# Kernel tuning notes

Hardware: AMD Instinct MI355X
Metric: run time of the kernel (lower is better)

Reference implementation:

```python
import jax, jax.numpy as jnp
import numpy as np

D_MODEL = 1024
NUM_HEADS = 16
HEAD_DIM = D_MODEL // NUM_HEADS
ALPHA = 1.0


def setup_inputs() -> dict:
    key = jax.random.key(0)
    ks = jax.random.split(key, 9)
    B, T, D = 2, 2048, D_MODEL
    s = 1.0 / np.sqrt(D)
    inp = {
        "x": jax.random.normal(ks[0], (B, T, D), dtype=jnp.float32),
        "Wq": jax.random.uniform(ks[1], (D, D), jnp.float32, -s, s),
        "bq": jax.random.uniform(ks[2], (D,), jnp.float32, -s, s),
        "Wk": jax.random.uniform(ks[3], (D, D), jnp.float32, -s, s),
        "bk": jax.random.uniform(ks[4], (D,), jnp.float32, -s, s),
        "Wv": jax.random.uniform(ks[5], (D, D), jnp.float32, -s, s),
        "bv": jax.random.uniform(ks[6], (D,), jnp.float32, -s, s),
        "Wo": jax.random.uniform(ks[7], (D, D), jnp.float32, -s, s),
        "bo": jax.random.uniform(ks[8], (D,), jnp.float32, -s, s),
    }
    return inp


def reference(x, Wq, bq, Wk, bk, Wv, bv, Wo, bo):
    B, T, D = x.shape
    H, hd = NUM_HEADS, HEAD_DIM

    def split_heads(y):  # [B,T,D] -> [B,H,T,hd]
        return y.reshape(B, T, H, hd).transpose(0, 2, 1, 3)

    Q = split_heads(x @ Wq.T + bq)
    K = split_heads(x @ Wk.T + bk)
    V = split_heads(x @ Wv.T + bv)

    scores = jnp.einsum('bhid,bhjd->bhij', Q, K) / jnp.sqrt(jnp.float32(hd))

    t = jnp.arange(T)
    delta = t[:, None] - t[None, :]  # [T,T], i - j
    causal_mask = delta < 0          # j > i (strict upper triangle)
    # similarity_power_law decay bias: -(delta)^alpha for delta >= 0, else 0
    decay = jnp.where(causal_mask, 0.0, -(delta.astype(jnp.float32) ** ALPHA))

    scores = jnp.where(causal_mask, -jnp.inf, scores) + decay
    attn = jax.nn.softmax(scores, axis=-1)

    out = jnp.einsum('bhij,bhjd->bhid', attn, V)
    out = out.transpose(0, 2, 1, 3).reshape(B, T, D)
    return out @ Wo.T + bo
```

## Files before the change

### kernel.cpp

```cpp
#include <hip/hip_runtime.h>

#define TT 2048
#define DD 1024
#define HH 16
#define HD 64

typedef __bf16 bf16x8 __attribute__((ext_vector_type(8)));
typedef short short4v __attribute__((ext_vector_type(4)));
typedef float f32x4 __attribute__((ext_vector_type(4)));
typedef unsigned short ushort8v __attribute__((ext_vector_type(8)));

__device__ __forceinline__ unsigned short f2bf(float f) {
  unsigned u = __float_as_uint(f);
  u += 0x7fffu + ((u >> 16) & 1u);
  return (unsigned short)(u >> 16);
}

#if __has_builtin(__builtin_amdgcn_mfma_f32_16x16x16bf16_1k)
__device__ __forceinline__ f32x4 mfma16(short4v a, short4v b, f32x4 c) {
  return __builtin_amdgcn_mfma_f32_16x16x16bf16_1k(a, b, c, 0, 0, 0);
}
#else
__device__ __forceinline__ f32x4 mfma16(short4v a, short4v b, f32x4 c) {
  asm("v_mfma_f32_16x16x16_bf16 %0, %1, %2, %0\n\ts_nop 7\n\ts_nop 7"
      : "+v"(c) : "v"(a), "v"(b));
  return c;
}
#endif

typedef void __attribute__((address_space(1))) as1_void;
typedef void __attribute__((address_space(3))) as3_void;
__device__ __forceinline__ void gl_lds16(const void* g, void* l) {
  __builtin_amdgcn_global_load_lds((as1_void*)g, (as3_void*)l, 16, 0, 0);
}

__global__ __launch_bounds__(256)
void wcmha_cast_all(const float4* __restrict__ x,  const float4* __restrict__ wq,
                    const float4* __restrict__ wk, const float4* __restrict__ wv,
                    const float4* __restrict__ wo,
                    ushort8v* __restrict__ xb,  ushort8v* __restrict__ wqb,
                    ushort8v* __restrict__ wkb, ushort8v* __restrict__ wvb,
                    ushort8v* __restrict__ wob) {
  const int i = blockIdx.x * 256 + threadIdx.x;
  const float4* src;
  ushort8v* dst;
  int off;
  if (i < 524288) {
    src = x; dst = xb; off = i;
  } else {
    int j = i - 524288;
    int sel = j >> 17;
    off = j & 131071;
    const float4* ws_[4] = {wq, wk, wv, wo};
    ushort8v* wd_[4] = {wqb, wkb, wvb, wob};
    src = ws_[sel]; dst = wd_[sel];
  }
  float4 a = src[off * 2];
  float4 b = src[off * 2 + 1];
  ushort8v o;
  o[0] = f2bf(a.x); o[1] = f2bf(a.y); o[2] = f2bf(a.z); o[3] = f2bf(a.w);
  o[4] = f2bf(b.x); o[5] = f2bf(b.y); o[6] = f2bf(b.z); o[7] = f2bf(b.w);
  dst[off] = o;
}

template <int BN_, bool SWAP>
__device__ __forceinline__ void gemm_db(const unsigned short* __restrict__ X,
                                        const unsigned short* __restrict__ W,
                                        int m0, int n0,
                                        unsigned short* As, unsigned short* Bs,
                                        f32x4 acc[4][BN_ / 32]) {
  constexpr int NI = BN_ / 32;
  constexpr int JB = (BN_ * 4) / 256;
  const int tid = threadIdx.x, wid = tid >> 6, lane = tid & 63;
  const int m = lane & 15, quad = lane >> 4;
  const int wm = (wid >> 1) * 64, wn = (wid & 1) * (BN_ / 2);
  const int xq = (quad ^ ((m >> 1) & 3)) * 8;

  const unsigned short* gA[2];
  const unsigned short* gB[JB];
#pragma unroll
  for (int j = 0; j < 2; ++j) {
    int c = wid * 64 + lane + j * 256;
    gA[j] = X + (size_t)(m0 + (c >> 2)) * DD + ((c & 3) ^ ((c >> 3) & 3)) * 8;
  }
#pragma unroll
  for (int j = 0; j < JB; ++j) {
    int c = wid * 64 + lane + j * 256;
    gB[j] = W + (size_t)(n0 + (c >> 2)) * DD + ((c & 3) ^ ((c >> 3) & 3)) * 8;
  }
  unsigned short* lA[2][2];
  unsigned short* lB[2][JB];
#pragma unroll
  for (int p = 0; p < 2; ++p) {
#pragma unroll
    for (int j = 0; j < 2; ++j)
      lA[p][j] = As + p * (128 * 32) + (wid * 64 + j * 256) * 8;
#pragma unroll
    for (int j = 0; j < JB; ++j)
      lB[p][j] = Bs + p * (BN_ * 32) + (wid * 64 + j * 256) * 8;
  }

#pragma unroll
  for (int i = 0; i < 4; ++i)
#pragma unroll
    for (int j = 0; j < NI; ++j) acc[i][j] = (f32x4){0.f, 0.f, 0.f, 0.f};

#pragma unroll
  for (int j = 0; j < 2; ++j) gl_lds16(gA[j], lA[0][j]);
#pragma unroll
  for (int j = 0; j < JB; ++j) gl_lds16(gB[j], lB[0][j]);

  for (int k = 0; k < 32; ++k) {
    const int p = k & 1;
    __syncthreads();
    if (k < 31) {
      const int k1 = (k + 1) * 32;
#pragma unroll
      for (int j = 0; j < 2; ++j) gl_lds16(gA[j] + k1, lA[p ^ 1][j]);
#pragma unroll
      for (int j = 0; j < JB; ++j) gl_lds16(gB[j] + k1, lB[p ^ 1][j]);
    }
    const unsigned short* ap = As + p * (128 * 32);
    const unsigned short* bp = Bs + p * (BN_ * 32);
    bf16x8 af[4], bf[NI];
#pragma unroll
    for (int mi = 0; mi < 4; ++mi)
      af[mi] = *(const bf16x8*)&ap[(wm + mi * 16 + m) * 32 + xq];
#pragma unroll
    for (int ni = 0; ni < NI; ++ni)
      bf[ni] = *(const bf16x8*)&bp[(wn + ni * 16 + m) * 32 + xq];
#pragma unroll
    for (int mi = 0; mi < 4; ++mi)
#pragma unroll
      for (int ni = 0; ni < NI; ++ni)
        acc[mi][ni] = SWAP
            ? __builtin_amdgcn_mfma_f32_16x16x32_bf16(bf[ni], af[mi], acc[mi][ni], 0, 0, 0)
            : __builtin_amdgcn_mfma_f32_16x16x32_bf16(af[mi], bf[ni], acc[mi][ni], 0, 0, 0);
  }
}

__global__ __launch_bounds__(512, 2)
void wcmha_qkv8(const unsigned short* __restrict__ X,
                const unsigned short* __restrict__ WQKV,
                const float* __restrict__ bq, const float* __restrict__ bk,
                const float* __restrict__ bv,
                unsigned short* __restrict__ Qb,
                unsigned short* __restrict__ Kb,
                unsigned short* __restrict__ Vt) {
  __shared__ unsigned short As[2 * 2 * 256 * 32];
  __shared__ unsigned short Bs[2 * 2 * 256 * 32];
  const int tid = threadIdx.x;
  const int lane = tid & 63, wid = tid >> 6;
  const int m = lane & 15, quad = lane >> 4;
  const int wr = wid >> 2, wc = wid & 3;

  const int mt = blockIdx.x & 15, nt = blockIdx.x >> 4;
  const int m0 = mt * 256;
  const int mat = nt >> 2;
  const int n0w = nt * 256;
  const int n0l = (nt & 3) * 256;

  const int srow = tid >> 2;
  const int schunk = ((tid & 3) ^ ((tid >> 3) & 3)) * 8;
  const unsigned short* gA0 = X + (size_t)(m0 + srow) * DD + schunk;
  const unsigned short* gA1 = gA0 + (size_t)128 * DD;
  const unsigned short* gB0 = WQKV + (size_t)(n0w + srow) * DD + schunk;
  const unsigned short* gB1 = gB0 + (size_t)128 * DD;
  const int ldst = tid * 8;

#define SA(buf, ks, koff)                                                     \
  {                                                                           \
    gl_lds16(gA0 + (koff), &As[((buf) * 2 + (ks)) * 8192 + ldst]);            \
    gl_lds16(gA1 + (koff), &As[((buf) * 2 + (ks)) * 8192 + 4096 + ldst]);     \
  }
#define SB(buf, ks, koff)                                                     \
  {                                                                           \
    gl_lds16(gB0 + (koff), &Bs[((buf) * 2 + (ks)) * 8192 + ldst]);            \
    gl_lds16(gB1 + (koff), &Bs[((buf) * 2 + (ks)) * 8192 + 4096 + ldst]);     \
  }

  f32x4 acc[8][4];
#pragma unroll
  for (int i = 0; i < 8; ++i)
#pragma unroll
    for (int j = 0; j < 4; ++j) acc[i][j] = (f32x4){0.f, 0.f, 0.f, 0.f};

  SA(0, 0, 0) SB(0, 0, 0)
  SA(0, 1, 32) SB(0, 1, 32)
  SA(1, 0, 64) SB(1, 0, 64)

  const int xq = (quad ^ ((m >> 1) & 3)) * 8;
  const int arow = wr * 128 + m;
  const int brow = wc * 64 + m;

#pragma unroll 1
  for (int kt = 0; kt < 16; ++kt) {
    const int cur = kt & 1, nxt = cur ^ 1;
    const unsigned short* a0 = &As[(cur * 2 + 0) * 8192];
    const unsigned short* b0 = &Bs[(cur * 2 + 0) * 8192];
    const unsigned short* a1 = &As[(cur * 2 + 1) * 8192];
    const unsigned short* b1 = &Bs[(cur * 2 + 1) * 8192];
    bf16x8 af[8], bf[4];

    if (kt < 15) { asm volatile("s_waitcnt vmcnt(8)" ::: "memory"); }
    else         { asm volatile("s_waitcnt vmcnt(4)" ::: "memory"); }
    __builtin_amdgcn_s_barrier();
    __builtin_amdgcn_sched_barrier(0);
#pragma unroll
    for (int mi = 0; mi < 8; ++mi)
      af[mi] = *(const bf16x8*)&a0[(arow + mi * 16) * 32 + xq];
#pragma unroll
    for (int ni = 0; ni < 4; ++ni)
      bf[ni] = *(const bf16x8*)&b0[(brow + ni * 16) * 32 + xq];
    if (kt < 15) { const int kA = (kt + 1) * 64 + 32; SA(nxt, 1, kA) SB(nxt, 1, kA) }
    __builtin_amdgcn_s_setprio(1);
#pragma unroll
    for (int mi = 0; mi < 8; ++mi)
#pragma unroll
      for (int ni = 0; ni < 4; ++ni)
        acc[mi][ni] = __builtin_amdgcn_mfma_f32_16x16x32_bf16(bf[ni], af[mi], acc[mi][ni], 0, 0, 0);
    __builtin_amdgcn_s_setprio(0);

    if (kt < 15) { asm volatile("s_waitcnt vmcnt(8)" ::: "memory"); }
    else         { asm volatile("s_waitcnt vmcnt(0)" ::: "memory"); }
    __builtin_amdgcn_s_barrier();
    __builtin_amdgcn_sched_barrier(0);
#pragma unroll
    for (int mi = 0; mi < 8; ++mi)
      af[mi] = *(const bf16x8*)&a1[(arow + mi * 16) * 32 + xq];
#pragma unroll
    for (int ni = 0; ni < 4; ++ni)
      bf[ni] = *(const bf16x8*)&b1[(brow + ni * 16) * 32 + xq];
    if (kt < 14) { const int kB = (kt + 2) * 64; SA(cur, 0, kB) SB(cur, 0, kB) }
    __builtin_amdgcn_s_setprio(1);
#pragma unroll
    for (int mi = 0; mi < 8; ++mi)
#pragma unroll
      for (int ni = 0; ni < 4; ++ni)
        acc[mi][ni] = __builtin_amdgcn_mfma_f32_16x16x32_bf16(bf[ni], af[mi], acc[mi][ni], 0, 0, 0);
    __builtin_amdgcn_s_setprio(0);
  }
#undef SA
#undef SB

  if (mat < 2) {
    const float* bias = mat ? bk : bq;
    unsigned short* dst = mat ? Kb : Qb;
#pragma unroll
    for (int mi = 0; mi < 8; ++mi) {
      int row = m0 + wr * 128 + mi * 16 + m;
      int b = row >> 11, t = row & (TT - 1);
#pragma unroll
      for (int ni = 0; ni < 4; ++ni) {
        int col0 = n0l + wc * 64 + ni * 16 + quad * 4;
        int h = col0 >> 6, d0 = col0 & 63;
        float4 bb = *(const float4*)&bias[col0];
        short4v v;
        v[0] = (short)f2bf(acc[mi][ni][0] + bb.x);
        v[1] = (short)f2bf(acc[mi][ni][1] + bb.y);
        v[2] = (short)f2bf(acc[mi][ni][2] + bb.z);
        v[3] = (short)f2bf(acc[mi][ni][3] + bb.w);
        *(short4v*)&dst[((size_t)(b * HH + h) * TT + t) * HD + d0] = v;
      }
    }
  } else {
#pragma unroll
    for (int mi = 0; mi < 8; ++mi) {
      int row = m0 + wr * 128 + mi * 16 + m;
      int b = row >> 11, t = row & (TT - 1);
#pragma unroll
      for (int ni = 0; ni < 4; ++ni) {
        int col0 = n0l + wc * 64 + ni * 16 + quad * 4;
        int h = col0 >> 6, d0 = col0 & 63;
#pragma unroll
        for (int r = 0; r < 4; ++r) {
          float bb = bv[col0 + r];
          Vt[((size_t)(b * HH + h) * HD + d0 + r) * TT + t] =
              f2bf(acc[mi][ni][r] + bb);
        }
      }
    }
  }
}

__global__ __launch_bounds__(256)
void wcmha_gemm_out(const unsigned short* __restrict__ X,
                    const unsigned short* __restrict__ W,
                    const float* __restrict__ bias,
                    float* __restrict__ Y) {
  __shared__ unsigned short As[2 * 128 * 32];
  __shared__ unsigned short Bs[2 * 64 * 32];
  const int m0 = blockIdx.x * 128;
  const int n0 = blockIdx.y * 64;
  const int lane = threadIdx.x & 63, wid = threadIdx.x >> 6;
  const int m = lane & 15, quad = lane >> 4;
  const int wm = (wid >> 1) * 64, wn = (wid & 1) * 32;

  f32x4 acc[4][2];
  gemm_db<64, true>(X, W, m0, n0, As, Bs, acc);

#pragma unroll
  for (int mi = 0; mi < 4; ++mi) {
    int row = m0 + wm + mi * 16 + m;
#pragma unroll
    for (int ni = 0; ni < 2; ++ni) {
      int col0 = n0 + wn + ni * 16 + quad * 4;
      float4 bb = *(const float4*)&bias[col0];
      float4 o;
      o.x = acc[mi][ni][0] + bb.x;
      o.y = acc[mi][ni][1] + bb.y;
      o.z = acc[mi][ni][2] + bb.z;
      o.w = acc[mi][ni][3] + bb.w;
      *(float4*)&Y[(size_t)row * DD + col0] = o;
    }
  }
}

__global__ __launch_bounds__(256)
void wcmha_attn(const unsigned short* __restrict__ Qb,
                const unsigned short* __restrict__ Kb,
                const unsigned short* __restrict__ Vt,
                unsigned short* __restrict__ O) {
  const int wid = threadIdx.x >> 6, lane = threadIdx.x & 63;
  const int gw = (blockIdx.x << 2) + wid;
  const int qt = gw & 127, bh = gw >> 7;
  const int qbase = qt << 4;
  const int il = lane & 15, quad = lane >> 4;
  const int ig = qbase + il;

  const unsigned short* q_ptr = Qb + (size_t)bh * TT * HD;
  const unsigned short* k_ptr = Kb + (size_t)bh * TT * HD;
  const unsigned short* v_ptr = Vt + (size_t)bh * HD * TT;

  const bf16x8 qf0 = *(const bf16x8*)(q_ptr + (size_t)ig * HD + quad * 8);
  const bf16x8 qf1 = *(const bf16x8*)(q_ptr + (size_t)ig * HD + 32 + quad * 8);

  const int j0 = (qbase >= 32) ? qbase - 32 : 0;

  f32x4 st[3];
#pragma unroll
  for (int jt = 0; jt < 3; ++jt) {
    const unsigned short* kp = k_ptr + (size_t)(j0 + jt * 16 + il) * HD;
    bf16x8 k0 = *(const bf16x8*)(kp + quad * 8);
    bf16x8 k1 = *(const bf16x8*)(kp + 32 + quad * 8);
    f32x4 a = {0.f, 0.f, 0.f, 0.f};
    a = __builtin_amdgcn_mfma_f32_16x16x32_bf16(k0, qf0, a, 0, 0, 0);
    a = __builtin_amdgcn_mfma_f32_16x16x32_bf16(k1, qf1, a, 0, 0, 0);
    st[jt] = a;
  }

  float mloc = -3.0e38f;
#pragma unroll
  for (int jt = 0; jt < 3; ++jt)
#pragma unroll
    for (int r = 0; r < 4; ++r) {
      int jg = j0 + jt * 16 + quad * 4 + r;
      float v = (jg > ig) ? -3.0e38f : st[jt][r] * 0.125f - (float)(ig - jg);
      st[jt][r] = v;
      mloc = fmaxf(mloc, v);
    }
  mloc = fmaxf(mloc, __shfl_xor(mloc, 16));
  mloc = fmaxf(mloc, __shfl_xor(mloc, 32));

  float rs = 0.f;
  short4v pf[3];
#pragma unroll
  for (int jt = 0; jt < 3; ++jt)
#pragma unroll
    for (int r = 0; r < 4; ++r) {
      float p = __expf(st[jt][r] - mloc);
      rs += p;
      pf[jt][r] = (short)f2bf(p);
    }
  rs += __shfl_xor(rs, 16);
  rs += __shfl_xor(rs, 32);

  f32x4 o_acc[4];
#pragma unroll
  for (int nt = 0; nt < 4; ++nt) o_acc[nt] = (f32x4){0.f, 0.f, 0.f, 0.f};
#pragma unroll
  for (int jt = 0; jt < 3; ++jt)
#pragma unroll
    for (int nt = 0; nt < 4; ++nt) {
      short4v vf = *(const short4v*)(v_ptr + (size_t)(nt * 16 + il) * TT +
                                     j0 + jt * 16 + quad * 4);
      o_acc[nt] = mfma16(vf, pf[jt], o_acc[nt]);
    }

  const float inv_l = 1.f / rs;
  const int b = bh >> 4, hh = bh & 15;
  unsigned short* ob = O + ((size_t)(b * TT + ig)) * DD + hh * HD;
#pragma unroll
  for (int nt = 0; nt < 4; ++nt) {
    short4v v;
#pragma unroll
    for (int r = 0; r < 4; ++r) v[r] = (short)f2bf(o_acc[nt][r] * inv_l);
    *(short4v*)&ob[nt * 16 + quad * 4] = v;
  }
}

extern "C" void kernel_launch(void* const* d_in, const int* in_sizes, int n_in,
                              void* d_out, int out_size, void* d_ws, size_t ws_size,
                              hipStream_t stream) {
  const float* x  = (const float*)d_in[0];
  const float* Wq = (const float*)d_in[1];
  const float* bq = (const float*)d_in[2];
  const float* Wk = (const float*)d_in[3];
  const float* bk = (const float*)d_in[4];
  const float* Wv = (const float*)d_in[5];
  const float* bv = (const float*)d_in[6];
  const float* Wo = (const float*)d_in[7];
  const float* bo = (const float*)d_in[8];

  char* ws = (char*)d_ws;
  unsigned short* xb  = (unsigned short*)(ws);
  unsigned short* wqb = (unsigned short*)(ws + (8u << 20));
  unsigned short* wkb = wqb + (1u << 20);
  unsigned short* wvb = wkb + (1u << 20);
  unsigned short* wob = wvb + (1u << 20);
  unsigned short* Qb  = (unsigned short*)(ws + (16u << 20));
  unsigned short* Kb  = (unsigned short*)(ws + (24u << 20));
  unsigned short* Vt  = (unsigned short*)(ws + (32u << 20));
  unsigned short* Ob  = xb;

  wcmha_cast_all<<<4096, 256, 0, stream>>>(
      (const float4*)x, (const float4*)Wq, (const float4*)Wk,
      (const float4*)Wv, (const float4*)Wo,
      (ushort8v*)xb, (ushort8v*)wqb, (ushort8v*)wkb, (ushort8v*)wvb,
      (ushort8v*)wob);

  wcmha_qkv8<<<192, 512, 0, stream>>>(xb, wqb, bq, bk, bv, Qb, Kb, Vt);

  wcmha_attn<<<1024, 256, 0, stream>>>(Qb, Kb, Vt, Ob);

  wcmha_gemm_out<<<dim3(32, 16), 256, 0, stream>>>(Ob, wob, bo, (float*)d_out);
}
```

Measured before the change: 159.6 us.

## Restructure QKV GEMM main loop into four-phase pipeline with 64-wide K tiles

The fused QKV projection GEMM now stages 256x64 K-tiles (double-buffered) instead of pairs of 32-wide sub-tiles, using an 8-chunk XOR swizzle in shared memory. Each K iteration is split into four MFMA phases, each with half the A fragments (4 instead of 8), which lowers register pressure. Global-to-LDS loads for the next tile are interleaved across the phases. This aims to overlap loading with compute more evenly and cut VGPR use, at the cost of more barriers and lgkmcnt waits per iteration.

```diff
diff --git a/kernel.cpp b/kernel.cpp
--- a/kernel.cpp
+++ b/kernel.cpp
@@ -147,8 +147,8 @@
                 unsigned short* __restrict__ Qb,
                 unsigned short* __restrict__ Kb,
                 unsigned short* __restrict__ Vt) {
-  __shared__ unsigned short As[2 * 2 * 256 * 32];
-  __shared__ unsigned short Bs[2 * 2 * 256 * 32];
+  __shared__ unsigned short As[2 * 256 * 64];
+  __shared__ unsigned short Bs[2 * 256 * 64];
   const int tid = threadIdx.x;
   const int lane = tid & 63, wid = tid >> 6;
   const int m = lane & 15, quad = lane >> 4;
@@ -160,23 +160,22 @@
   const int n0w = nt * 256;
   const int n0l = (nt & 3) * 256;
 
-  const int srow = tid >> 2;
-  const int schunk = ((tid & 3) ^ ((tid >> 3) & 3)) * 8;
-  const unsigned short* gA0 = X + (size_t)(m0 + srow) * DD + schunk;
-  const unsigned short* gA1 = gA0 + (size_t)128 * DD;
-  const unsigned short* gB0 = WQKV + (size_t)(n0w + srow) * DD + schunk;
-  const unsigned short* gB1 = gB0 + (size_t)128 * DD;
-  const int ldst = tid * 8;
-
-#define SA(buf, ks, koff)                                                     \
+  const int srow = tid >> 3;
+  const int sch8 = ((tid & 7) ^ (srow & 7)) * 8;
+  const unsigned short* gA = X + (size_t)(m0 + srow) * DD + sch8;
+  const unsigned short* gB = WQKV + (size_t)(n0w + srow) * DD + sch8;
+  unsigned short* lA = As + tid * 8;
+  unsigned short* lB = Bs + tid * 8;
+
+#define SA2(p, c0_, c1_, koff)                                                \
   {                                                                           \
-    gl_lds16(gA0 + (koff), &As[((buf) * 2 + (ks)) * 8192 + ldst]);            \
-    gl_lds16(gA1 + (koff), &As[((buf) * 2 + (ks)) * 8192 + 4096 + ldst]);     \
-  }
-#define SB(buf, ks, koff)                                                     \
+    gl_lds16(gA + (c0_) * (64 * DD) + (koff), lA + (p) * 16384 + (c0_) * 4096); \
+    gl_lds16(gA + (c1_) * (64 * DD) + (koff), lA + (p) * 16384 + (c1_) * 4096); \
+  }
+#define SB2(p, c0_, c1_, koff)                                                \
   {                                                                           \
-    gl_lds16(gB0 + (koff), &Bs[((buf) * 2 + (ks)) * 8192 + ldst]);            \
-    gl_lds16(gB1 + (koff), &Bs[((buf) * 2 + (ks)) * 8192 + 4096 + ldst]);     \
+    gl_lds16(gB + (c0_) * (64 * DD) + (koff), lB + (p) * 16384 + (c0_) * 4096); \
+    gl_lds16(gB + (c1_) * (64 * DD) + (koff), lB + (p) * 16384 + (c1_) * 4096); \
   }
 
   f32x4 acc[8][4];
@@ -185,63 +184,96 @@
 #pragma unroll
     for (int j = 0; j < 4; ++j) acc[i][j] = (f32x4){0.f, 0.f, 0.f, 0.f};
 
-  SA(0, 0, 0) SB(0, 0, 0)
-  SA(0, 1, 32) SB(0, 1, 32)
-  SA(1, 0, 64) SB(1, 0, 64)
-
-  const int xq = (quad ^ ((m >> 1) & 3)) * 8;
-  const int arow = wr * 128 + m;
-  const int brow = wc * 64 + m;
+  SB2(0, 0, 1, 0) SB2(0, 2, 3, 0) SA2(0, 0, 2, 0) SA2(0, 1, 3, 0)
+
+  const int arow_e = (wr * 128 + m) * 64;
+  const int brow_e = (wc * 64 + m) * 64;
+  const int ch0 = (quad ^ (m & 7)) * 8;
+  const int ch1 = ((4 | quad) ^ (m & 7)) * 8;
 
 #pragma unroll 1
   for (int kt = 0; kt < 16; ++kt) {
     const int cur = kt & 1, nxt = cur ^ 1;
-    const unsigned short* a0 = &As[(cur * 2 + 0) * 8192];
-    const unsigned short* b0 = &Bs[(cur * 2 + 0) * 8192];
-    const unsigned short* a1 = &As[(cur * 2 + 1) * 8192];
-    const unsigned short* b1 = &Bs[(cur * 2 + 1) * 8192];
-    bf16x8 af[8], bf[4];
-
-    if (kt < 15) { asm volatile("s_waitcnt vmcnt(8)" ::: "memory"); }
-    else         { asm volatile("s_waitcnt vmcnt(4)" ::: "memory"); }
-    __builtin_amdgcn_s_barrier();
-    __builtin_amdgcn_sched_barrier(0);
-#pragma unroll
-    for (int mi = 0; mi < 8; ++mi)
-      af[mi] = *(const bf16x8*)&a0[(arow + mi * 16) * 32 + xq];
+    const unsigned short* ab = &As[cur * 16384];
+    const unsigned short* bb = &Bs[cur * 16384];
+    const int koffN = (kt + 1) * 64;
+    bf16x8 af[4], bf[4];
+
+    asm volatile("s_waitcnt vmcnt(2)" ::: "memory");
+    __builtin_amdgcn_s_barrier();
+    __builtin_amdgcn_sched_barrier(0);
+#pragma unroll
+    for (int mi = 0; mi < 4; ++mi)
+      af[mi] = *(const bf16x8*)&ab[arow_e + mi * 1024 + ch0];
 #pragma unroll
     for (int ni = 0; ni < 4; ++ni)
-      bf[ni] = *(const bf16x8*)&b0[(brow + ni * 16) * 32 + xq];
-    if (kt < 15) { const int kA = (kt + 1) * 64 + 32; SA(nxt, 1, kA) SB(nxt, 1, kA) }
+      bf[ni] = *(const bf16x8*)&bb[brow_e + ni * 1024 + ch0];
+    if (kt < 15) SB2(nxt, 0, 1, koffN)
+    __builtin_amdgcn_s_barrier();
+    asm volatile("s_waitcnt lgkmcnt(0)" ::: "memory");
+    __builtin_amdgcn_sched_barrier(0);
     __builtin_amdgcn_s_setprio(1);
 #pragma unroll
-    for (int mi = 0; mi < 8; ++mi)
+    for (int mi = 0; mi < 4; ++mi)
 #pragma unroll
       for (int ni = 0; ni < 4; ++ni)
         acc[mi][ni] = __builtin_amdgcn_mfma_f32_16x16x32_bf16(bf[ni], af[mi], acc[mi][ni], 0, 0, 0);
     __builtin_amdgcn_s_setprio(0);
 
-    if (kt < 15) { asm volatile("s_waitcnt vmcnt(8)" ::: "memory"); }
+    if (kt < 15) { asm volatile("s_waitcnt vmcnt(2)" ::: "memory"); }
     else         { asm volatile("s_waitcnt vmcnt(0)" ::: "memory"); }
     __builtin_amdgcn_s_barrier();
     __builtin_amdgcn_sched_barrier(0);
 #pragma unroll
-    for (int mi = 0; mi < 8; ++mi)
-      af[mi] = *(const bf16x8*)&a1[(arow + mi * 16) * 32 + xq];
+    for (int mi = 0; mi < 4; ++mi)
+      af[mi] = *(const bf16x8*)&ab[arow_e + (mi + 4) * 1024 + ch0];
+    if (kt < 15) SB2(nxt, 2, 3, koffN)
+    __builtin_amdgcn_s_barrier();
+    asm volatile("s_waitcnt lgkmcnt(0)" ::: "memory");
+    __builtin_amdgcn_sched_barrier(0);
+    __builtin_amdgcn_s_setprio(1);
+#pragma unroll
+    for (int mi = 0; mi < 4; ++mi)
+#pragma unroll
+      for (int ni = 0; ni < 4; ++ni)
+        acc[mi + 4][ni] = __builtin_amdgcn_mfma_f32_16x16x32_bf16(bf[ni], af[mi], acc[mi + 4][ni], 0, 0, 0);
+    __builtin_amdgcn_s_setprio(0);
+
+#pragma unroll
+    for (int mi = 0; mi < 4; ++mi)
+      af[mi] = *(const bf16x8*)&ab[arow_e + mi * 1024 + ch1];
 #pragma unroll
     for (int ni = 0; ni < 4; ++ni)
-      bf[ni] = *(const bf16x8*)&b1[(brow + ni * 16) * 32 + xq];
-    if (kt < 14) { const int kB = (kt + 2) * 64; SA(cur, 0, kB) SB(cur, 0, kB) }
+      bf[ni] = *(const bf16x8*)&bb[brow_e + ni * 1024 + ch1];
+    if (kt < 15) SA2(nxt, 0, 2, koffN)
+    __builtin_amdgcn_s_barrier();
+    asm volatile("s_waitcnt lgkmcnt(0)" ::: "memory");
+    __builtin_amdgcn_sched_barrier(0);
     __builtin_amdgcn_s_setprio(1);
 #pragma unroll
-    for (int mi = 0; mi < 8; ++mi)
+    for (int mi = 0; mi < 4; ++mi)
 #pragma unroll
       for (int ni = 0; ni < 4; ++ni)
         acc[mi][ni] = __builtin_amdgcn_mfma_f32_16x16x32_bf16(bf[ni], af[mi], acc[mi][ni], 0, 0, 0);
     __builtin_amdgcn_s_setprio(0);
-  }
-#undef SA
-#undef SB
+
+#pragma unroll
+    for (int mi = 0; mi < 4; ++mi)
+      af[mi] = *(const bf16x8*)&ab[arow_e + (mi + 4) * 1024 + ch1];
+    if (kt < 15) SA2(nxt, 1, 3, koffN)
+    __builtin_amdgcn_s_barrier();
+    asm volatile("s_waitcnt lgkmcnt(0)" ::: "memory");
+    __builtin_amdgcn_sched_barrier(0);
+    __builtin_amdgcn_s_setprio(1);
+#pragma unroll
+    for (int mi = 0; mi < 4; ++mi)
+#pragma unroll
+      for (int ni = 0; ni < 4; ++ni)
+        acc[mi + 4][ni] = __builtin_amdgcn_mfma_f32_16x16x32_bf16(bf[ni], af[mi], acc[mi + 4][ni], 0, 0, 0);
+    __builtin_amdgcn_s_setprio(0);
+  }
+#undef SA2
+#undef SB2
 
   if (mat < 2) {
     const float* bias = mat ? bk : bq;
@@ -254,12 +286,12 @@
       for (int ni = 0; ni < 4; ++ni) {
         int col0 = n0l + wc * 64 + ni * 16 + quad * 4;
         int h = col0 >> 6, d0 = col0 & 63;
-        float4 bb = *(const float4*)&bias[col0];
+        float4 bb2 = *(const float4*)&bias[col0];
         short4v v;
-        v[0] = (short)f2bf(acc[mi][ni][0] + bb.x);
-        v[1] = (short)f2bf(acc[mi][ni][1] + bb.y);
-        v[2] = (short)f2bf(acc[mi][ni][2] + bb.z);
-        v[3] = (short)f2bf(acc[mi][ni][3] + bb.w);
+        v[0] = (short)f2bf(acc[mi][ni][0] + bb2.x);
+        v[1] = (short)f2bf(acc[mi][ni][1] + bb2.y);
+        v[2] = (short)f2bf(acc[mi][ni][2] + bb2.z);
+        v[3] = (short)f2bf(acc[mi][ni][3] + bb2.w);
         *(short4v*)&dst[((size_t)(b * HH + h) * TT + t) * HD + d0] = v;
       }
     }
@@ -274,9 +306,9 @@
         int h = col0 >> 6, d0 = col0 & 63;
 #pragma unroll
         for (int r = 0; r < 4; ++r) {
-          float bb = bv[col0 + r];
+          float bb2 = bv[col0 + r];
           Vt[((size_t)(b * HH + h) * HD + d0 + r) * TT + t] =
-              f2bf(acc[mi][ni][r] + bb);
+              f2bf(acc[mi][ni][r] + bb2);
         }
       }
     }
```

After: 160.8 us. Within noise of the previous version (+0.7%).
